# Optimization experiments

Hardware: AMD Instinct MI355X
Metric: run time of the kernel (lower is better)

## Reference

```python
import jax, jax.numpy as jnp
import numpy as np

NUM_EXPERTS = 64
TOPK = 8
EPS = 1.1920929e-07  # torch.finfo(float32).eps


def setup_inputs() -> dict:
    key = jax.random.key(0)
    k1, k2 = jax.random.split(key)
    hidden_states = jax.random.normal(k1, (1, 4096, 4096), dtype=jnp.float32)
    wg_weight = jax.random.normal(k2, (NUM_EXPERTS, 4096), dtype=jnp.float32) * 0.02
    return {"hidden_states": hidden_states, "wg_weight": wg_weight}


def _routing(logits, capacity):
    # logits: [T, E]; capacity: static python int
    gates = jax.nn.softmax(logits, axis=1)                       # [T, E]
    _, idx = jax.lax.top_k(gates, TOPK)                          # [T, k]
    emask = jax.nn.one_hot(idx, NUM_EXPERTS, dtype=jnp.float32)  # [T, k, E]
    # sum of selected gate probs per token, clamped at fp32 eps
    gates_s = jnp.clip(jnp.einsum('tke,te->t', emask, gates), EPS)[:, None]
    router_probs = gates / gates_s                               # [T, E]
    # priority: cumulative position of each token within each expert,
    # scanned over (topk-major, token-minor) flattened order
    idx_flat = idx.T.reshape(-1)                                 # [k*T]
    mflat = jax.nn.one_hot(idx_flat, NUM_EXPERTS, dtype=jnp.int32)
    tp = jnp.cumsum(mflat, axis=0) * mflat - 1                   # [k*T, E]
    tp = tp.reshape(TOPK, -1, NUM_EXPERTS).transpose(1, 0, 2).max(axis=1)  # [T, E]
    valid = (tp >= 0) & (tp < capacity)                          # [T, E]
    tp = jnp.where(valid, tp, 0)
    dispatch_mask = jax.nn.one_hot(tp, capacity, dtype=jnp.bool_) & valid[:, :, None]  # [T, E, C]
    combine_weights = router_probs[:, :, None] * dispatch_mask   # [T, E, C]
    return combine_weights, dispatch_mask


def reference(hidden_states, wg_weight):
    b, s, h = hidden_states.shape
    x = hidden_states.reshape(-1, h).astype(jnp.float32)         # [T, H]
    logits = x @ wg_weight.T                                     # [T, E]
    # expert_capacity = max tokens assigned to any expert (data-dependent,
    # computed eagerly as in the torch .item() call)
    _, idx = jax.lax.top_k(jax.nn.softmax(logits, axis=1), TOPK)
    counts = jnp.bincount(idx.reshape(-1), length=NUM_EXPERTS)
    capacity = int(counts.max())
    return _routing(logits, capacity)
```

## Files before the change

### kernel.cpp

```cpp
#include <hip/hip_runtime.h>
#include <hip/hip_bf16.h>


#define TOK 4096
#define HID 4096
#define NE  64
#define NK  8
#define NSPLIT 8

typedef __attribute__((ext_vector_type(8))) short short8;
typedef __attribute__((ext_vector_type(4))) float f32x4;

__device__ __forceinline__ short f2bf(float f) {
  __hip_bfloat16 h = __float2bfloat16(f);
  return *reinterpret_cast<short*>(&h);
}
__device__ __forceinline__ float bf2f(short s) {
  unsigned u = ((unsigned)(unsigned short)s) << 16;
  return __uint_as_float(u);
}
__device__ __forceinline__ void cvt3(float f, short& s0, short& s1, short& s2) {
  s0 = f2bf(f);
  float r1 = f - bf2f(s0);
  s1 = f2bf(r1);
  float r2 = r1 - bf2f(s1);
  s2 = f2bf(r2);
}

__global__ __launch_bounds__(256) void mega(
    const float* __restrict__ x, const float* __restrict__ wg,
    double* __restrict__ partial, int kchunk, int ngemm, int nfill,
    float* __restrict__ out, int out_n) {
  const int bx  = blockIdx.x;
  const int tid = threadIdx.x;

  if (bx >= ngemm) {
    const int    fid    = bx - ngemm;
    const size_t n4     = ((size_t)(unsigned)out_n) >> 2;
    const size_t stride = (size_t)nfill * 256;
    f32x4* o4 = (f32x4*)out;
    const f32x4 z4 = (f32x4){0.f, 0.f, 0.f, 0.f};
    size_t i = (size_t)fid * 256 + tid;
    for (; i + 3 * stride < n4; i += 4 * stride) {
      o4[i]              = z4;
      o4[i + stride]     = z4;
      o4[i + 2 * stride] = z4;
      o4[i + 3 * stride] = z4;
    }
    for (; i < n4; i += stride) o4[i] = z4;
    if (fid == 0 && tid == 0)
      for (size_t i2 = n4 << 2; i2 < (size_t)(unsigned)out_n; ++i2) out[i2] = 0.f;
    return;
  }

  __shared__ __align__(16) short XA[3][64][72];
  __shared__ __align__(16) short WB[3][64][72];
  const int tileid = bx & 63;
  const int slab   = bx >> 6;
  const int t0   = tileid * 64;
  const int k0   = slab * kchunk;
  const int lane = tid & 63;
  const int w    = tid >> 6;
  const int m    = lane & 15;
  const int q    = lane >> 4;
  const int lrow = tid >> 2;
  const int lq   = tid & 3;

  f32x4 acc[4];
#pragma unroll
  for (int nt = 0; nt < 4; ++nt) acc[nt] = (f32x4){0.f, 0.f, 0.f, 0.f};

  for (int s = 0; s < kchunk; s += 64) {
    const int kk = k0 + s;
#pragma unroll
    for (int c = 0; c < 4; ++c) {
      const int col = lq * 16 + c * 4;
      float4 xv = *(const float4*)&x [(size_t)(t0 + lrow) * HID + kk + col];
      float4 wv = *(const float4*)&wg[(size_t)lrow * HID + kk + col];
      short4 p0, p1, p2;
      cvt3(xv.x, p0.x, p1.x, p2.x);  cvt3(xv.y, p0.y, p1.y, p2.y);
      cvt3(xv.z, p0.z, p1.z, p2.z);  cvt3(xv.w, p0.w, p1.w, p2.w);
      *(short4*)&XA[0][lrow][col] = p0;
      *(short4*)&XA[1][lrow][col] = p1;
      *(short4*)&XA[2][lrow][col] = p2;
      cvt3(wv.x, p0.x, p1.x, p2.x);  cvt3(wv.y, p0.y, p1.y, p2.y);
      cvt3(wv.z, p0.z, p1.z, p2.z);  cvt3(wv.w, p0.w, p1.w, p2.w);
      *(short4*)&WB[0][lrow][col] = p0;
      *(short4*)&WB[1][lrow][col] = p1;
      *(short4*)&WB[2][lrow][col] = p2;
    }
    __syncthreads();
#pragma unroll
    for (int kc = 0; kc < 64; kc += 32) {
      short8 a0 = *(const short8*)&XA[0][w * 16 + m][kc + q * 8];
      short8 a1 = *(const short8*)&XA[1][w * 16 + m][kc + q * 8];
      short8 a2 = *(const short8*)&XA[2][w * 16 + m][kc + q * 8];
#pragma unroll
      for (int nt = 0; nt < 4; ++nt) {
        short8 b0 = *(const short8*)&WB[0][nt * 16 + m][kc + q * 8];
        short8 b1 = *(const short8*)&WB[1][nt * 16 + m][kc + q * 8];
        short8 b2 = *(const short8*)&WB[2][nt * 16 + m][kc + q * 8];
        acc[nt] = __builtin_amdgcn_mfma_f32_16x16x32_bf16(a0, b0, acc[nt], 0, 0, 0);
        acc[nt] = __builtin_amdgcn_mfma_f32_16x16x32_bf16(a0, b1, acc[nt], 0, 0, 0);
        acc[nt] = __builtin_amdgcn_mfma_f32_16x16x32_bf16(a1, b0, acc[nt], 0, 0, 0);
        acc[nt] = __builtin_amdgcn_mfma_f32_16x16x32_bf16(a0, b2, acc[nt], 0, 0, 0);
        acc[nt] = __builtin_amdgcn_mfma_f32_16x16x32_bf16(a1, b1, acc[nt], 0, 0, 0);
        acc[nt] = __builtin_amdgcn_mfma_f32_16x16x32_bf16(a2, b0, acc[nt], 0, 0, 0);
      }
    }
    __syncthreads();
  }

  double* base = partial + (size_t)slab * TOK * NE;
#pragma unroll
  for (int nt = 0; nt < 4; ++nt)
#pragma unroll
    for (int v = 0; v < 4; ++v)
      base[(size_t)(t0 + w * 16 + q * 4 + v) * NE + nt * 16 + m] =
          (double)acc[nt][v];
}

__global__ __launch_bounds__(256) void topk_kernel(
    const double* __restrict__ partial, int nsplit,
    int* __restrict__ idx_kt, float* __restrict__ w_kt) {
  const int gid  = blockIdx.x * blockDim.x + threadIdx.x;
  const int t    = gid >> 6;
  const int lane = gid & 63;

  double v = 0.0;
  for (int p = 0; p < nsplit; ++p)
    v += partial[(size_t)p * TOK * NE + (size_t)t * NE + lane];

  double m = v;
#pragma unroll
  for (int off = 32; off; off >>= 1) {
    double o = __shfl_xor(m, off);
    m = o > m ? o : m;
  }
  double g = exp(v - m);
  double s = g;
#pragma unroll
  for (int off = 32; off; off >>= 1) s += __shfl_xor(s, off);
  double gate = g / s;

  float key = (float)gate;
  double ssel = 0.0;
  int my_k = -1;
#pragma unroll
  for (int k = 0; k < NK; ++k) {
    float bv = key;
    int   bi = lane;
#pragma unroll
    for (int off = 32; off; off >>= 1) {
      float ov = __shfl_xor(bv, off);
      int   oi = __shfl_xor(bi, off);
      if (ov > bv || (ov == bv && oi < bi)) { bv = ov; bi = oi; }
    }
    ssel += __shfl(gate, bi);
    if (lane == bi) { my_k = k; key = -1.0f; }
  }
  double gs = ssel;
  const double eps = (double)1.1920929e-07f;
  if (gs < eps) gs = eps;

  if (my_k >= 0) {
    idx_kt[my_k * TOK + t] = lane;
    w_kt [my_k * TOK + t] = (float)(gate / gs);
  }
}

__global__ __launch_bounds__(1024) void rank_scatter(
    const int* __restrict__ idx_kt, const float* __restrict__ w_kt,
    float* __restrict__ out, int C) {
  const int e    = blockIdx.x;
  const int tid  = threadIdx.x;
  const int lane = tid & 63;
  const int w    = tid >> 6;
  __shared__ int wt[16];
  int running = 0;
  const unsigned long long below = (1ull << lane) - 1ull;

  for (int i0 = 0; i0 < NK * TOK; i0 += 1024) {
    const int i = i0 + tid;
    const bool mhit = (idx_kt[i] == e);
    unsigned long long mask = __ballot(mhit);
    if (lane == 0) wt[w] = __popcll(mask);
    __syncthreads();
    int woff = 0, tot = 0;
#pragma unroll
    for (int j = 0; j < 16; ++j) {
      int c = wt[j];
      tot += c;
      if (j < w) woff += c;
    }
    if (mhit) {
      const int c = running + woff + __popcll(mask & below);
      if (c < C) {
        const int t = i & (TOK - 1);
        size_t off = ((size_t)t * NE + e) * (size_t)C + (size_t)c;
        out[off] = w_kt[i];
        out[(size_t)TOK * NE * C + off] = 1.0f;
      }
    }
    running += tot;
    __syncthreads();
  }
}

extern "C" void kernel_launch(void* const* d_in, const int* in_sizes, int n_in,
                              void* d_out, int out_size, void* d_ws, size_t ws_size,
                              hipStream_t stream) {
  const float* x  = (const float*)d_in[0];
  const float* wg = (const float*)d_in[1];
  float* out = (float*)d_out;

  const int C = out_size / (2 * TOK * NE);

  char* ws = (char*)d_ws;
  double* partial = (double*)ws;
  const size_t psz = (size_t)NSPLIT * TOK * NE * sizeof(double);
  int*    idx_kt  = (int*)  (ws + psz);
  float*  w_kt    = (float*)(ws + psz + (size_t)NK * TOK * sizeof(int));

  const int kchunk = HID / NSPLIT;
  const int ngemm  = 64 * NSPLIT;
  const int nfill  = 2048;

  mega        <<<ngemm + nfill, 256, 0, stream>>>(x, wg, partial, kchunk,
                                                  ngemm, nfill, out, out_size);
  topk_kernel <<<TOK * 64 / 256, 256, 0, stream>>>(partial, NSPLIT, idx_kt, w_kt);
  rank_scatter<<<NE, 1024, 0, stream>>>(idx_kt, w_kt, out, C);
}
```

Baseline: 1.270 ms.

## Split zero-fill from GEMM and stage a copy of x in workspace

Separates the fused fill+GEMM kernel into a fill kernel that also copies x into workspace and a separate 2D-grid GEMM kernel that reads the copy. The intent appears to be warming x in the last-level cache so the GEMM reads hit cache. It adds a full extra read and write of x and removes the overlap between the output zero-fill and the GEMM.

```diff
diff --git a/kernel.cpp b/kernel.cpp
--- a/kernel.cpp
+++ b/kernel.cpp
@@ -27,38 +27,47 @@
   s2 = f2bf(r2);
 }
 
-__global__ __launch_bounds__(256) void mega(
-    const float* __restrict__ x, const float* __restrict__ wg,
-    double* __restrict__ partial, int kchunk, int ngemm, int nfill,
-    float* __restrict__ out, int out_n) {
+__global__ __launch_bounds__(256) void fill_copy(
+    const float* __restrict__ x, float* __restrict__ xcopy, int ncopy,
+    int nfill, float* __restrict__ out, int out_n) {
   const int bx  = blockIdx.x;
   const int tid = threadIdx.x;
 
-  if (bx >= ngemm) {
-    const int    fid    = bx - ngemm;
-    const size_t n4     = ((size_t)(unsigned)out_n) >> 2;
-    const size_t stride = (size_t)nfill * 256;
-    f32x4* o4 = (f32x4*)out;
-    const f32x4 z4 = (f32x4){0.f, 0.f, 0.f, 0.f};
-    size_t i = (size_t)fid * 256 + tid;
-    for (; i + 3 * stride < n4; i += 4 * stride) {
-      o4[i]              = z4;
-      o4[i + stride]     = z4;
-      o4[i + 2 * stride] = z4;
-      o4[i + 3 * stride] = z4;
-    }
-    for (; i < n4; i += stride) o4[i] = z4;
-    if (fid == 0 && tid == 0)
-      for (size_t i2 = n4 << 2; i2 < (size_t)(unsigned)out_n; ++i2) out[i2] = 0.f;
+  if (bx < ncopy) {
+    const size_t nf4    = (size_t)TOK * HID / 4;
+    const size_t stride = (size_t)ncopy * 256;
+    const f32x4* x4 = (const f32x4*)x;
+    f32x4* c4 = (f32x4*)xcopy;
+    for (size_t i = (size_t)bx * 256 + tid; i < nf4; i += stride)
+      c4[i] = x4[i];
     return;
   }
 
+  const int    fid    = bx - ncopy;
+  const size_t n4     = ((size_t)(unsigned)out_n) >> 2;
+  const size_t stride = (size_t)nfill * 256;
+  f32x4* o4 = (f32x4*)out;
+  const f32x4 z4 = (f32x4){0.f, 0.f, 0.f, 0.f};
+  size_t i = (size_t)fid * 256 + tid;
+  for (; i + 3 * stride < n4; i += 4 * stride) {
+    o4[i]              = z4;
+    o4[i + stride]     = z4;
+    o4[i + 2 * stride] = z4;
+    o4[i + 3 * stride] = z4;
+  }
+  for (; i < n4; i += stride) o4[i] = z4;
+  if (fid == 0 && tid == 0)
+    for (size_t i2 = n4 << 2; i2 < (size_t)(unsigned)out_n; ++i2) out[i2] = 0.f;
+}
+
+__global__ __launch_bounds__(256) void gemm_bf16x3(
+    const float* __restrict__ x, const float* __restrict__ wg,
+    double* __restrict__ partial, int kchunk) {
   __shared__ __align__(16) short XA[3][64][72];
   __shared__ __align__(16) short WB[3][64][72];
-  const int tileid = bx & 63;
-  const int slab   = bx >> 6;
-  const int t0   = tileid * 64;
-  const int k0   = slab * kchunk;
+  const int tid = threadIdx.x;
+  const int t0   = blockIdx.x * 64;
+  const int k0   = blockIdx.y * kchunk;
   const int lane = tid & 63;
   const int w    = tid >> 6;
   const int m    = lane & 15;
@@ -111,7 +120,7 @@
     __syncthreads();
   }
 
-  double* base = partial + (size_t)slab * TOK * NE;
+  double* base = partial + (size_t)blockIdx.y * TOK * NE;
 #pragma unroll
   for (int nt = 0; nt < 4; ++nt)
 #pragma unroll
@@ -216,18 +225,27 @@
 
   const int C = out_size / (2 * TOK * NE);
 
+  const size_t psz    = (size_t)NSPLIT * TOK * NE * sizeof(double);
+  const size_t tailsz = 2 * (size_t)NK * TOK * sizeof(int);
+  const size_t xsz    = (size_t)TOK * HID * sizeof(float);
+
   char* ws = (char*)d_ws;
   double* partial = (double*)ws;
-  const size_t psz = (size_t)NSPLIT * TOK * NE * sizeof(double);
   int*    idx_kt  = (int*)  (ws + psz);
   float*  w_kt    = (float*)(ws + psz + (size_t)NK * TOK * sizeof(int));
-
+  const size_t xoff = (psz + tailsz + 255) & ~(size_t)255;
+  const bool   have_copy = (xoff + xsz) <= ws_size;
+  float* xcopy = have_copy ? (float*)(ws + xoff) : nullptr;
+
+  const int ncopy = have_copy ? 256 : 0;
+  const int nfill = 2048;
   const int kchunk = HID / NSPLIT;
-  const int ngemm  = 64 * NSPLIT;
-  const int nfill  = 2048;
-
-  mega        <<<ngemm + nfill, 256, 0, stream>>>(x, wg, partial, kchunk,
-                                                  ngemm, nfill, out, out_size);
+  const float* xsrc = have_copy ? xcopy : x;
+
+  fill_copy   <<<ncopy + nfill, 256, 0, stream>>>(x, xcopy, ncopy, nfill,
+                                                  out, out_size);
+  dim3 bgrid(TOK / 64, NSPLIT);
+  gemm_bf16x3 <<<bgrid, 256, 0, stream>>>(xsrc, wg, partial, kchunk);
   topk_kernel <<<TOK * 64 / 256, 256, 0, stream>>>(partial, NSPLIT, idx_kt, w_kt);
   rank_scatter<<<NE, 1024, 0, stream>>>(idx_kt, w_kt, out, C);
 }
```

Result: no change. 1.292 ms (+1.7%).

## Replace per-chunk ballot rank loop with per-thread bitmask and block scan

Applied to the files above, without the earlier changes.

The topk kernel now stores indices and weights token-major ([T][8]) instead of k-major. The scatter kernel has each of 1024 threads own 32 consecutive (k, token) slots. Each thread builds a hit bitmask, runs a single Hillis-Steele prefix scan in shared memory, then writes its hits sequentially. This removes the 32 loop iterations, each with two barriers, that the old ballot-based ranking needed per expert. In exchange, reads are strided by 8 ints per token, so the gather is less coalesced, and the writes from each thread become serial.

```diff
diff --git a/kernel.cpp b/kernel.cpp
--- a/kernel.cpp
+++ b/kernel.cpp
@@ -122,7 +122,7 @@
 
 __global__ __launch_bounds__(256) void topk_kernel(
     const double* __restrict__ partial, int nsplit,
-    int* __restrict__ idx_kt, float* __restrict__ w_kt) {
+    int* __restrict__ idx8, float* __restrict__ w8) {
   const int gid  = blockIdx.x * blockDim.x + threadIdx.x;
   const int t    = gid >> 6;
   const int lane = gid & 63;
@@ -164,46 +164,51 @@
   if (gs < eps) gs = eps;
 
   if (my_k >= 0) {
-    idx_kt[my_k * TOK + t] = lane;
-    w_kt [my_k * TOK + t] = (float)(gate / gs);
-  }
-}
-
-__global__ __launch_bounds__(1024) void rank_scatter(
-    const int* __restrict__ idx_kt, const float* __restrict__ w_kt,
+    idx8[t * 8 + my_k] = lane;
+    w8 [t * 8 + my_k] = (float)(gate / gs);
+  }
+}
+
+__global__ __launch_bounds__(1024) void scatter2(
+    const int* __restrict__ idx8, const float* __restrict__ w8,
     float* __restrict__ out, int C) {
-  const int e    = blockIdx.x;
-  const int tid  = threadIdx.x;
-  const int lane = tid & 63;
-  const int w    = tid >> 6;
-  __shared__ int wt[16];
-  int running = 0;
-  const unsigned long long below = (1ull << lane) - 1ull;
-
-  for (int i0 = 0; i0 < NK * TOK; i0 += 1024) {
-    const int i = i0 + tid;
-    const bool mhit = (idx_kt[i] == e);
-    unsigned long long mask = __ballot(mhit);
-    if (lane == 0) wt[w] = __popcll(mask);
+  const int e   = blockIdx.x;
+  const int tid = threadIdx.x;
+  __shared__ int sa[1024];
+  __shared__ int sb[1024];
+
+  const int base = tid * 32;
+  const int k    = base >> 12;
+  const int tbase = base & (TOK - 1);
+  unsigned mask = 0u;
+  int cnt = 0;
+#pragma unroll 8
+  for (int s = 0; s < 32; ++s) {
+    if (idx8[(tbase + s) * 8 + k] == e) { mask |= (1u << s); ++cnt; }
+  }
+
+  sa[tid] = cnt;
+  __syncthreads();
+  int* src = sa; int* dst = sb;
+  for (int off = 1; off < 1024; off <<= 1) {
+    int v = src[tid];
+    if (tid >= off) v += src[tid - off];
+    dst[tid] = v;
     __syncthreads();
-    int woff = 0, tot = 0;
-#pragma unroll
-    for (int j = 0; j < 16; ++j) {
-      int c = wt[j];
-      tot += c;
-      if (j < w) woff += c;
-    }
-    if (mhit) {
-      const int c = running + woff + __popcll(mask & below);
-      if (c < C) {
-        const int t = i & (TOK - 1);
-        size_t off = ((size_t)t * NE + e) * (size_t)C + (size_t)c;
-        out[off] = w_kt[i];
-        out[(size_t)TOK * NE * C + off] = 1.0f;
-      }
-    }
-    running += tot;
-    __syncthreads();
+    int* tmp = src; src = dst; dst = tmp;
+  }
+  int c = src[tid] - cnt;
+
+  for (unsigned mm = mask; mm; mm &= (mm - 1)) {
+    const int s = __builtin_ctz(mm);
+    const int t = tbase + s;
+    if (c < C) {
+      const float wv = w8[t * 8 + k];
+      const size_t off2 = ((size_t)t * NE + e) * (size_t)C + (size_t)c;
+      out[off2] = wv;
+      out[(size_t)TOK * NE * C + off2] = 1.0f;
+    }
+    ++c;
   }
 }
 
@@ -219,15 +224,15 @@
   char* ws = (char*)d_ws;
   double* partial = (double*)ws;
   const size_t psz = (size_t)NSPLIT * TOK * NE * sizeof(double);
-  int*    idx_kt  = (int*)  (ws + psz);
-  float*  w_kt    = (float*)(ws + psz + (size_t)NK * TOK * sizeof(int));
+  int*    idx8 = (int*)  (ws + psz);
+  float*  w8   = (float*)(ws + psz + (size_t)NK * TOK * sizeof(int));
 
   const int kchunk = HID / NSPLIT;
   const int ngemm  = 64 * NSPLIT;
   const int nfill  = 2048;
 
-  mega        <<<ngemm + nfill, 256, 0, stream>>>(x, wg, partial, kchunk,
-                                                  ngemm, nfill, out, out_size);
-  topk_kernel <<<TOK * 64 / 256, 256, 0, stream>>>(partial, NSPLIT, idx_kt, w_kt);
-  rank_scatter<<<NE, 1024, 0, stream>>>(idx_kt, w_kt, out, C);
-}
+  mega       <<<ngemm + nfill, 256, 0, stream>>>(x, wg, partial, kchunk,
+                                                 ngemm, nfill, out, out_size);
+  topk_kernel<<<TOK * 64 / 256, 256, 0, stream>>>(partial, NSPLIT, idx8, w8);
+  scatter2   <<<NE, 1024, 0, stream>>>(idx8, w8, out, C);
+}
```

Result: no change. 1.268 ms (-0.2%).
